# Kernel optimization log

Hardware: AMD Instinct MI355X
Metric: run time of the kernel (lower is better)

The kernel has to match this reference:

```python
import jax, jax.numpy as jnp
import numpy as np

NU, NI, E = 100000, 50000, 819200
FIN, H, OUT = 128, 32, 32


def _l2norm(x):
    # F.normalize(x, p=2, dim=-1): divide by max(||x||, 1e-12)
    n = jnp.linalg.norm(x, axis=-1, keepdims=True)
    return x / jnp.maximum(n, 1e-12)


def _sage(x_src, x_dst, src, dst, n_dst, wl, b, wr):
    # PyG SAGEConv(mean aggr, normalize=True):
    # out = l2norm(lin_l(mean_j x_src[j]) + lin_r(x_dst))
    msg = x_src[src]                                   # [E, Fin] gather
    agg = jax.ops.segment_sum(msg, dst, num_segments=n_dst)
    cnt = jax.ops.segment_sum(jnp.ones((src.shape[0],), x_src.dtype), dst,
                              num_segments=n_dst)
    mean = agg / jnp.maximum(cnt, 1.0)[:, None]
    return _l2norm(mean @ wl.T + b + x_dst @ wr.T)


def setup_inputs() -> dict:
    key = jax.random.key(0)
    ks = jax.random.split(key, 24)
    d = {}
    d["x_user"] = jax.random.normal(ks[0], (NU, FIN), jnp.float32)
    d["x_item"] = jax.random.normal(ks[1], (NI, FIN), jnp.float32)
    d["edge_user"] = jax.random.randint(ks[2], (E,), 0, NU, jnp.int32)
    d["edge_item"] = jax.random.randint(ks[3], (E,), 0, NI, jnp.int32)
    i = [4]
    def w(shape):
        a = jax.random.normal(ks[i[0]], shape, jnp.float32) * 0.05
        i[0] += 1
        return a
    d["wl0_ui"] = w((H, FIN)); d["b0_ui"] = w((H,)); d["wr0_ui"] = w((H, FIN))
    d["wl0_iu"] = w((H, FIN)); d["b0_iu"] = w((H,)); d["wr0_iu"] = w((H, FIN))
    d["wl1_ui"] = w((H, H)); d["b1_ui"] = w((H,)); d["wr1_ui"] = w((H, H))
    d["wl1_iu"] = w((H, H)); d["b1_iu"] = w((H,)); d["wr1_iu"] = w((H, H))
    d["wp_user"] = w((OUT, H)); d["bp_user"] = w((OUT,))
    d["wp_item"] = w((OUT, H)); d["bp_item"] = w((OUT,))
    return d


def reference(x_user, x_item, edge_user, edge_item,
              wl0_ui, b0_ui, wr0_ui, wl0_iu, b0_iu, wr0_iu,
              wl1_ui, b1_ui, wr1_ui, wl1_iu, b1_iu, wr1_iu,
              wp_user, bp_user, wp_item, bp_item):
    # layer 0 (inference mode: dropout is identity)
    item1 = jax.nn.relu(_sage(x_user, x_item, edge_user, edge_item, NI,
                              wl0_ui, b0_ui, wr0_ui))
    user1 = jax.nn.relu(_sage(x_item, x_user, edge_item, edge_user, NU,
                              wl0_iu, b0_iu, wr0_iu))
    # layer 1
    item2 = jax.nn.relu(_sage(user1, item1, edge_user, edge_item, NI,
                              wl1_ui, b1_ui, wr1_ui))
    user2 = jax.nn.relu(_sage(item1, user1, edge_item, edge_user, NU,
                              wl1_iu, b1_iu, wr1_iu))
    user_emb = _l2norm(user2 @ wp_user.T + bp_user)
    item_emb = _l2norm(item2 @ wp_item.T + bp_item)
    return (user_emb, item_emb)
```

## Files before the change

### kernel.cpp

```cpp
#include <hip/hip_runtime.h>
#include <hip/hip_fp16.h>

#define NU 100000
#define NI 50000
#define NE 819200
#define FIN 128
#define HH 32

#define NCH 200
#define NBU 98
#define NBI 49

#define G_P0I 6250
#define G_P0U 12500
#define G_P1U 782
#define G_P1I 391


__global__ void cnt1_k(const int4* __restrict__ eu4, const int4* __restrict__ ei4,
                       int* __restrict__ cntU, int* __restrict__ cntI) {
    __shared__ unsigned cnt[128];
    int b = blockIdx.x;
    int c, NB;
    const int4* D;
    int* M;
    if (b < NCH) { c = b; D = eu4; M = cntU; NB = NBU; }
    else         { c = b - NCH; D = ei4; M = cntI; NB = NBI; }
    int tid = threadIdx.x;
    if (tid < 128) cnt[tid] = 0u;
    __syncthreads();
    int base = c * 1024;
#pragma unroll
    for (int it = 0; it < 4; ++it) {
        int4 v = D[base + it * 256 + tid];
        atomicAdd(&cnt[v.x >> 10], 1u);
        atomicAdd(&cnt[v.y >> 10], 1u);
        atomicAdd(&cnt[v.z >> 10], 1u);
        atomicAdd(&cnt[v.w >> 10], 1u);
    }
    __syncthreads();
    for (int i = tid; i < NB; i += 256) M[i * NCH + c] = (int)cnt[i];
}

__global__ __launch_bounds__(1024) void scan2_k(int* __restrict__ aU, int nU,
                                                int* __restrict__ aI, int nI) {
    __shared__ int ts[1024];
    int t = threadIdx.x;
    for (int pass = 0; pass < 2; ++pass) {
        int* a = pass ? aI : aU;
        int n  = pass ? nI : nU;
        int nper = (n + 1023) / 1024;
        int beg = t * nper;
        int end = beg + nper; if (end > n) end = n;
        int s = 0;
        for (int i = beg; i < end; ++i) s += a[i];
        ts[t] = s;
        __syncthreads();
        int incl = s;
        for (int off = 1; off < 1024; off <<= 1) {
            int y = (t >= off) ? ts[t - off] : 0;
            __syncthreads();
            incl += y;
            ts[t] = incl;
            __syncthreads();
        }
        int run = incl - s;
        for (int i = beg; i < end; ++i) { int v = a[i]; a[i] = run; run += v; }
        __syncthreads();
    }
}

__global__ void part_k(const int4* __restrict__ eu4, const int4* __restrict__ ei4,
                       const int* __restrict__ cntU, const int* __restrict__ cntI,
                       int2* __restrict__ partU, int2* __restrict__ partI) {
    __shared__ unsigned cur[128];
    int b = blockIdx.x;
    int c, NB;
    const int4 *D, *P;
    const int* M;
    int2* out;
    if (b < NCH) { c = b; D = eu4; P = ei4; M = cntU; out = partU; NB = NBU; }
    else         { c = b - NCH; D = ei4; P = eu4; M = cntI; out = partI; NB = NBI; }
    int tid = threadIdx.x;
    for (int i = tid; i < NB; i += 256) cur[i] = (unsigned)M[i * NCH + c];
    __syncthreads();
    int base = c * 1024;
#pragma unroll
    for (int it = 0; it < 4; ++it) {
        int4 d = D[base + it * 256 + tid];
        int4 p = P[base + it * 256 + tid];
        unsigned s;
        s = atomicAdd(&cur[d.x >> 10], 1u); out[s] = make_int2(d.x, p.x);
        s = atomicAdd(&cur[d.y >> 10], 1u); out[s] = make_int2(d.y, p.y);
        s = atomicAdd(&cur[d.z >> 10], 1u); out[s] = make_int2(d.z, p.z);
        s = atomicAdd(&cur[d.w >> 10], 1u); out[s] = make_int2(d.w, p.w);
    }
}

__global__ __launch_bounds__(1024) void build_k(const int2* __restrict__ partU,
                                                const int2* __restrict__ partI,
                                                const int* __restrict__ cntU,
                                                const int* __restrict__ cntI,
                                                int* __restrict__ rsU, int* __restrict__ rsI,
                                                int* __restrict__ csrU, int* __restrict__ csrI) {
    __shared__ unsigned dcnt[1024];
    __shared__ unsigned sc_[1024];
    int b = blockIdx.x;
    const int2* part;
    const int* M;
    int *rs, *csr;
    int bi, N, NB;
    if (b < NBU) { bi = b; part = partU; M = cntU; rs = rsU; csr = csrU; N = NU; NB = NBU; }
    else         { bi = b - NBU; part = partI; M = cntI; rs = rsI; csr = csrI; N = NI; NB = NBI; }
    int lo = bi * 1024;
    int bktbase = M[bi * NCH];
    int bktend = (bi + 1 < NB) ? M[(bi + 1) * NCH] : NE;
    int t = threadIdx.x;
    dcnt[t] = 0u;
    __syncthreads();
    for (int j = bktbase + t; j < bktend; j += 1024) {
        int2 p = part[j];
        atomicAdd(&dcnt[p.x - lo], 1u);
    }
    __syncthreads();
    unsigned cme = dcnt[t];
    sc_[t] = cme;
    __syncthreads();
    unsigned incl = cme;
    for (int off = 1; off < 1024; off <<= 1) {
        unsigned y = (t >= off) ? sc_[t - off] : 0u;
        __syncthreads();
        incl += y;
        sc_[t] = incl;
        __syncthreads();
    }
    unsigned excl = incl - cme;
    if (lo + t < N) rs[lo + t] = bktbase + (int)excl;
    if (bi == NB - 1 && t == 0) rs[N] = NE;
    __syncthreads();
    dcnt[t] = excl;
    __syncthreads();
    for (int j = bktbase + t; j < bktend; j += 1024) {
        int2 p = part[j];
        unsigned s = atomicAdd(&dcnt[p.x - lo], 1u);
        csr[bktbase + (int)s] = p.y;
    }
}

__device__ __forceinline__ void proj128_body(const float* __restrict__ X,
                                             const float* __restrict__ Wl,
                                             const float* __restrict__ Wr,
                                             __half* __restrict__ S, float* __restrict__ R,
                                             int N, int vb, float* sW) {
    int tid = threadIdx.x;
#pragma unroll
    for (int it = 0; it < 4; ++it) {
        int idx = it * 512 + tid;
        int col = idx & 63, k = (idx >> 6) * 4;
        const float* src = (col < 32) ? (Wl + col * FIN + k) : (Wr + (col - 32) * FIN + k);
        float4 w = *(const float4*)src;
        sW[(k + 0) * 68 + col] = w.x;
        sW[(k + 1) * 68 + col] = w.y;
        sW[(k + 2) * 68 + col] = w.z;
        sW[(k + 3) * 68 + col] = w.w;
    }
    __syncthreads();
    int ct = tid & 15, nt = tid >> 4;
    int c0 = ct * 4;
    int n0 = vb * 128 + nt * 4;
    int mA = n0 + 0; if (mA >= N) mA = N - 1;
    int mB = n0 + 1; if (mB >= N) mB = N - 1;
    int mC = n0 + 2; if (mC >= N) mC = N - 1;
    int mD = n0 + 3; if (mD >= N) mD = N - 1;
    const float* xA = X + (size_t)mA * FIN;
    const float* xB = X + (size_t)mB * FIN;
    const float* xC = X + (size_t)mC * FIN;
    const float* xD = X + (size_t)mD * FIN;
    float acc[4][4];
#pragma unroll
    for (int j = 0; j < 4; ++j)
#pragma unroll
        for (int i = 0; i < 4; ++i) acc[j][i] = 0.f;
#pragma unroll 4
    for (int k4 = 0; k4 < FIN; k4 += 4) {
        float4 a4 = *(const float4*)(xA + k4);
        float4 b4 = *(const float4*)(xB + k4);
        float4 c4 = *(const float4*)(xC + k4);
        float4 d4 = *(const float4*)(xD + k4);
        float xa[4] = {a4.x, a4.y, a4.z, a4.w};
        float xb[4] = {b4.x, b4.y, b4.z, b4.w};
        float xc[4] = {c4.x, c4.y, c4.z, c4.w};
        float xd[4] = {d4.x, d4.y, d4.z, d4.w};
#pragma unroll
        for (int kk = 0; kk < 4; ++kk) {
            float4 w = *(const float4*)&sW[(k4 + kk) * 68 + c0];
            acc[0][0] += xa[kk] * w.x; acc[0][1] += xa[kk] * w.y;
            acc[0][2] += xa[kk] * w.z; acc[0][3] += xa[kk] * w.w;
            acc[1][0] += xb[kk] * w.x; acc[1][1] += xb[kk] * w.y;
            acc[1][2] += xb[kk] * w.z; acc[1][3] += xb[kk] * w.w;
            acc[2][0] += xc[kk] * w.x; acc[2][1] += xc[kk] * w.y;
            acc[2][2] += xc[kk] * w.z; acc[2][3] += xc[kk] * w.w;
            acc[3][0] += xd[kk] * w.x; acc[3][1] += xd[kk] * w.y;
            acc[3][2] += xd[kk] * w.z; acc[3][3] += xd[kk] * w.w;
        }
    }
#pragma unroll
    for (int j = 0; j < 4; ++j) {
        int node = n0 + j;
        if (node < N) {
            if (c0 < 32) {
                __half2 h01 = __floats2half2_rn(acc[j][0], acc[j][1]);
                __half2 h23 = __floats2half2_rn(acc[j][2], acc[j][3]);
                __half2* dst = (__half2*)(S + (size_t)node * HH + c0);
                dst[0] = h01;
                dst[1] = h23;
            } else {
                float4 o;
                o.x = acc[j][0]; o.y = acc[j][1]; o.z = acc[j][2]; o.w = acc[j][3];
                *(float4*)(R + (size_t)node * HH + (c0 - 32)) = o;
            }
        }
    }
}

__global__ __launch_bounds__(512) void p1_k(const float* __restrict__ xu,
                                            const float* __restrict__ xi,
                                            const float* __restrict__ wl0_ui,
                                            const float* __restrict__ wr0_iu,
                                            const float* __restrict__ wl0_iu,
                                            const float* __restrict__ wr0_ui,
                                            __half* __restrict__ Su, float* __restrict__ Ru,
                                            __half* __restrict__ Si, float* __restrict__ Ri) {
    __shared__ float sW[128 * 68];
    int b = blockIdx.x;
    if (b < G_P1U) proj128_body(xu, wl0_ui, wr0_iu, Su, Ru, NU, b, sW);
    else           proj128_body(xi, wl0_iu, wr0_ui, Si, Ri, NI, b - G_P1U, sW);
}

__device__ __forceinline__ float4 gather4(const int* __restrict__ csr, int s0, int s1,
                                          const __half* __restrict__ S, int sc, int eh) {
    const char* Sb = (const char*)S;
    float4 acc = {0.f, 0.f, 0.f, 0.f};
    int j = s0 + eh;
    for (; j + 4 < s1; j += 8) {
        int i0 = csr[j], i1 = csr[j + 4];
        uint2 u0 = *(const uint2*)(Sb + ((size_t)i0 << 6) + sc * 8);
        uint2 u1 = *(const uint2*)(Sb + ((size_t)i1 << 6) + sc * 8);
        float2 f00 = __half22float2(*(__half2*)&u0.x);
        float2 f01 = __half22float2(*(__half2*)&u0.y);
        float2 f10 = __half22float2(*(__half2*)&u1.x);
        float2 f11 = __half22float2(*(__half2*)&u1.y);
        acc.x += f00.x + f10.x;
        acc.y += f00.y + f10.y;
        acc.z += f01.x + f11.x;
        acc.w += f01.y + f11.y;
    }
    if (j < s1) {
        int i0 = csr[j];
        uint2 u0 = *(const uint2*)(Sb + ((size_t)i0 << 6) + sc * 8);
        float2 f00 = __half22float2(*(__half2*)&u0.x);
        float2 f01 = __half22float2(*(__half2*)&u0.y);
        acc.x += f00.x; acc.y += f00.y; acc.z += f01.x; acc.w += f01.y;
    }
    acc.x += __shfl_xor(acc.x, 8);  acc.x += __shfl_xor(acc.x, 16);
    acc.y += __shfl_xor(acc.y, 8);  acc.y += __shfl_xor(acc.y, 16);
    acc.z += __shfl_xor(acc.z, 8);  acc.z += __shfl_xor(acc.z, 16);
    acc.w += __shfl_xor(acc.w, 8);  acc.w += __shfl_xor(acc.w, 16);
    return acc;
}

__global__ void p23_k(const int* __restrict__ csrI, const int* __restrict__ rsI,
                      const __half* __restrict__ Su, float* __restrict__ Ri,
                      const float* __restrict__ b0_ui,
                      const float* __restrict__ wl1_iu, const float* __restrict__ wr1_ui,
                      __half* __restrict__ Si2,
                      const int* __restrict__ csrU, const int* __restrict__ rsU,
                      const __half* __restrict__ Si, float* __restrict__ Ru,
                      const float* __restrict__ b0_iu,
                      const float* __restrict__ wl1_ui, const float* __restrict__ wr1_iu,
                      __half* __restrict__ Su2) {
    __shared__ float sWl[HH * 36];
    __shared__ float sWr[HH * 36];
    __shared__ float sH[8][36];
    int b = blockIdx.x;
    const int *csr, *rs;
    const __half* S;
    const float *bias, *Wl, *Wr;
    float* Rb;
    __half* S2;
    int vb;
    if (b < G_P0I) {
        csr = csrI; rs = rsI; S = Su; Rb = Ri; bias = b0_ui;
        Wl = wl1_iu; Wr = wr1_ui; S2 = Si2; vb = b;
    } else {
        csr = csrU; rs = rsU; S = Si; Rb = Ru; bias = b0_iu;
        Wl = wl1_ui; Wr = wr1_iu; S2 = Su2; vb = b - G_P0I;
    }
    int tid = threadIdx.x;
    {
        float4 a = ((const float4*)Wl)[tid];
        float4 w = ((const float4*)Wr)[tid];
        int e0 = tid * 4;
        int o = e0 >> 5, k = e0 & 31;
        sWl[(k + 0) * 36 + o] = a.x;
        sWl[(k + 1) * 36 + o] = a.y;
        sWl[(k + 2) * 36 + o] = a.z;
        sWl[(k + 3) * 36 + o] = a.w;
        sWr[(k + 0) * 36 + o] = w.x;
        sWr[(k + 1) * 36 + o] = w.y;
        sWr[(k + 2) * 36 + o] = w.z;
        sWr[(k + 3) * 36 + o] = w.w;
    }
    int g = tid >> 5;
    int lane5 = tid & 31;
    int sc = lane5 & 7, eh = lane5 >> 3;
    int n = vb * 8 + g;
    int s0 = rs[n], s1 = rs[n + 1];
    float4 acc = gather4(csr, s0, s1, S, sc, eh);
    float deg = (float)(s1 - s0);
    deg = deg > 1.f ? deg : 1.f;
    float4 r4 = *(const float4*)(Rb + (size_t)n * HH + 4 * sc);
    float4 b4 = *(const float4*)(bias + 4 * sc);
    float4 v4;
    v4.x = acc.x / deg + r4.x + b4.x;
    v4.y = acc.y / deg + r4.y + b4.y;
    v4.z = acc.z / deg + r4.z + b4.z;
    v4.w = acc.w / deg + r4.w + b4.w;
    float ss = v4.x * v4.x + v4.y * v4.y + v4.z * v4.z + v4.w * v4.w;
    ss += __shfl_xor(ss, 1);
    ss += __shfl_xor(ss, 2);
    ss += __shfl_xor(ss, 4);
    float nrm = sqrtf(ss);
    nrm = nrm > 1e-12f ? nrm : 1e-12f;
    v4.x /= nrm; v4.y /= nrm; v4.z /= nrm; v4.w /= nrm;
    v4.x = v4.x > 0.f ? v4.x : 0.f;
    v4.y = v4.y > 0.f ? v4.y : 0.f;
    v4.z = v4.z > 0.f ? v4.z : 0.f;
    v4.w = v4.w > 0.f ? v4.w : 0.f;
    if (eh == 0) {
        sH[g][4 * sc + 0] = v4.x;
        sH[g][4 * sc + 1] = v4.y;
        sH[g][4 * sc + 2] = v4.z;
        sH[g][4 * sc + 3] = v4.w;
    }
    __syncthreads();
    int c = tid & 31;
    float aL = 0.f, aR = 0.f;
#pragma unroll
    for (int k = 0; k < HH; ++k) {
        float x = sH[g][k];
        aL += x * sWl[k * 36 + c];
        aR += x * sWr[k * 36 + c];
    }
    S2[(size_t)n * HH + c] = __float2half_rn(aL);
    Rb[(size_t)n * HH + c] = aR;
}

__device__ __forceinline__ void pull1f_body(const int* __restrict__ csr,
                                            const int* __restrict__ rs,
                                            const __half* __restrict__ S,
                                            const float* __restrict__ R,
                                            const float* __restrict__ b1,
                                            const float* __restrict__ Wp,
                                            const float* __restrict__ bp,
                                            float* __restrict__ out, int vb, float* smem) {
    float* sWpT = smem;
    float* sH   = smem + HH * 36;
    int tid = threadIdx.x;
    {
        float4 a = ((const float4*)Wp)[tid];
        int e0 = tid * 4;
        int o = e0 >> 5, k = e0 & 31;
        sWpT[(k + 0) * 36 + o] = a.x;
        sWpT[(k + 1) * 36 + o] = a.y;
        sWpT[(k + 2) * 36 + o] = a.z;
        sWpT[(k + 3) * 36 + o] = a.w;
    }
    int g = tid >> 5;
    int lane5 = tid & 31;
    int sc = lane5 & 7, eh = lane5 >> 3;
    int n = vb * 8 + g;
    int s0 = rs[n], s1 = rs[n + 1];
    float4 acc = gather4(csr, s0, s1, S, sc, eh);
    float deg = (float)(s1 - s0);
    deg = deg > 1.f ? deg : 1.f;
    float4 r4 = *(const float4*)(R + (size_t)n * HH + 4 * sc);
    float4 b4 = *(const float4*)(b1 + 4 * sc);
    float4 v4;
    v4.x = acc.x / deg + r4.x + b4.x;
    v4.y = acc.y / deg + r4.y + b4.y;
    v4.z = acc.z / deg + r4.z + b4.z;
    v4.w = acc.w / deg + r4.w + b4.w;
    float ss = v4.x * v4.x + v4.y * v4.y + v4.z * v4.z + v4.w * v4.w;
    ss += __shfl_xor(ss, 1);
    ss += __shfl_xor(ss, 2);
    ss += __shfl_xor(ss, 4);
    float nrm = sqrtf(ss);
    nrm = nrm > 1e-12f ? nrm : 1e-12f;
    v4.x /= nrm; v4.y /= nrm; v4.z /= nrm; v4.w /= nrm;
    v4.x = v4.x > 0.f ? v4.x : 0.f;
    v4.y = v4.y > 0.f ? v4.y : 0.f;
    v4.z = v4.z > 0.f ? v4.z : 0.f;
    v4.w = v4.w > 0.f ? v4.w : 0.f;
    if (eh == 0) {
        sH[g * 36 + 4 * sc + 0] = v4.x;
        sH[g * 36 + 4 * sc + 1] = v4.y;
        sH[g * 36 + 4 * sc + 2] = v4.z;
        sH[g * 36 + 4 * sc + 3] = v4.w;
    }
    __syncthreads();
    int c = tid & 31;
    float a2f = bp[c];
#pragma unroll
    for (int k = 0; k < HH; ++k) a2f += sH[g * 36 + k] * sWpT[k * 36 + c];
    float s2 = a2f * a2f;
    s2 += __shfl_xor(s2, 1);
    s2 += __shfl_xor(s2, 2);
    s2 += __shfl_xor(s2, 4);
    s2 += __shfl_xor(s2, 8);
    s2 += __shfl_xor(s2, 16);
    float nrm2 = sqrtf(s2);
    nrm2 = nrm2 > 1e-12f ? nrm2 : 1e-12f;
    out[(size_t)n * HH + c] = a2f / nrm2;
}

__global__ void p4_k(const int* __restrict__ csrU, const int* __restrict__ rsU,
                     const __half* __restrict__ Si2, const float* __restrict__ Ru,
                     const float* __restrict__ b1_iu,
                     const float* __restrict__ wp_user, const float* __restrict__ bp_user,
                     const int* __restrict__ csrI, const int* __restrict__ rsI,
                     const __half* __restrict__ Su2, const float* __restrict__ Ri,
                     const float* __restrict__ b1_ui,
                     const float* __restrict__ wp_item, const float* __restrict__ bp_item,
                     float* __restrict__ out) {
    __shared__ float smem[HH * 36 + 8 * 36];
    int b = blockIdx.x;
    if (b < G_P0U) {
        pull1f_body(csrU, rsU, Si2, Ru, b1_iu, wp_user, bp_user, out, b, smem);
    } else {
        pull1f_body(csrI, rsI, Su2, Ri, b1_ui, wp_item, bp_item,
                    out + (size_t)NU * HH, b - G_P0U, smem);
    }
}


extern "C" void kernel_launch(void* const* d_in, const int* in_sizes, int n_in,
                              void* d_out, int out_size, void* d_ws, size_t ws_size,
                              hipStream_t stream) {
    const float* x_user = (const float*)d_in[0];
    const float* x_item = (const float*)d_in[1];
    const int* eu = (const int*)d_in[2];
    const int* ei = (const int*)d_in[3];
    const float* wl0_ui = (const float*)d_in[4];
    const float* b0_ui  = (const float*)d_in[5];
    const float* wr0_ui = (const float*)d_in[6];
    const float* wl0_iu = (const float*)d_in[7];
    const float* b0_iu  = (const float*)d_in[8];
    const float* wr0_iu = (const float*)d_in[9];
    const float* wl1_ui = (const float*)d_in[10];
    const float* b1_ui  = (const float*)d_in[11];
    const float* wr1_ui = (const float*)d_in[12];
    const float* wl1_iu = (const float*)d_in[13];
    const float* b1_iu  = (const float*)d_in[14];
    const float* wr1_iu = (const float*)d_in[15];
    const float* wp_user = (const float*)d_in[16];
    const float* bp_user = (const float*)d_in[17];
    const float* wp_item = (const float*)d_in[18];
    const float* bp_item = (const float*)d_in[19];
    float* out = (float*)d_out;
    (void)in_sizes; (void)n_in; (void)out_size; (void)ws_size;

    char* base = (char*)d_ws;
    size_t off = 0;
    auto take = [&](size_t bytes) -> size_t {
        size_t o = off;
        off += (bytes + 255) & ~(size_t)255;
        return o;
    };
    size_t o_rsU  = take((size_t)(NU + 1) * 4);
    size_t o_rsI  = take((size_t)(NI + 1) * 4);
    size_t o_cntU = take((size_t)NBU * NCH * 4);
    size_t o_cntI = take((size_t)NBI * NCH * 4);
    size_t o_csrU = take((size_t)NE * 4);
    size_t o_csrI = take((size_t)NE * 4);
    size_t o_partU = take((size_t)NE * 8);
    size_t o_partI = take((size_t)NE * 8);
    size_t o_Su = take((size_t)NU * HH * 2);
    size_t o_Si = take((size_t)NI * HH * 2);
    size_t o_Su2 = take((size_t)NU * HH * 2);
    size_t o_Si2 = take((size_t)NI * HH * 2);
    size_t o_Ru = take((size_t)NU * HH * 4);
    size_t o_Ri = take((size_t)NI * HH * 4);

    int* rsU  = (int*)(base + o_rsU);
    int* rsI  = (int*)(base + o_rsI);
    int* cntU = (int*)(base + o_cntU);
    int* cntI = (int*)(base + o_cntI);
    int* csrU = (int*)(base + o_csrU);
    int* csrI = (int*)(base + o_csrI);
    int2* partU = (int2*)(base + o_partU);
    int2* partI = (int2*)(base + o_partI);
    __half* Su = (__half*)(base + o_Su);
    __half* Si = (__half*)(base + o_Si);
    __half* Su2 = (__half*)(base + o_Su2);
    __half* Si2 = (__half*)(base + o_Si2);
    float* Ru = (float*)(base + o_Ru);
    float* Ri = (float*)(base + o_Ri);

    cnt1_k<<<2 * NCH, 256, 0, stream>>>((const int4*)eu, (const int4*)ei, cntU, cntI);
    scan2_k<<<1, 1024, 0, stream>>>(cntU, NBU * NCH, cntI, NBI * NCH);
    part_k<<<2 * NCH, 256, 0, stream>>>((const int4*)eu, (const int4*)ei,
                                        cntU, cntI, partU, partI);
    build_k<<<NBU + NBI, 1024, 0, stream>>>(partU, partI, cntU, cntI,
                                            rsU, rsI, csrU, csrI);

    p1_k<<<G_P1U + G_P1I, 512, 0, stream>>>(x_user, x_item, wl0_ui, wr0_iu,
                                            wl0_iu, wr0_ui, Su, Ru, Si, Ri);

    p23_k<<<G_P0I + G_P0U, 256, 0, stream>>>(csrI, rsI, Su, Ri, b0_ui, wl1_iu, wr1_ui, Si2,
                                             csrU, rsU, Si, Ru, b0_iu, wl1_ui, wr1_iu, Su2);

    p4_k<<<G_P0U + G_P0I, 256, 0, stream>>>(csrU, rsU, Si2, Ru, b1_iu, wp_user, bp_user,
                                            csrI, rsI, Su2, Ri, b1_ui, wp_item, bp_item,
                                            out);
}
```

Baseline: 223.1 us.

## Use MFMA fp16 instructions for layer-0 feature projection

Replaces the scalar FP32 shared-memory tiled projection (X @ [Wl;Wr]^T for 128-dim inputs) with a wave-per-16-row-tile kernel using mfma_f32_16x16x32_f16. Weights are held in registers as fp16 fragments and waves grid-stride over row tiles, with no shared memory or block sync. The projection is memory-bound on reading 150k x 128 floats, so the gain depends on how well the loads are issued. Inputs and weights are now rounded to fp16 before the multiply, which lowers precision, and the output stores become scattered scalar writes.

```diff
diff --git a/kernel.cpp b/kernel.cpp
--- a/kernel.cpp
+++ b/kernel.cpp
@@ -13,8 +13,11 @@
 
 #define G_P0I 6250
 #define G_P0U 12500
-#define G_P1U 782
-#define G_P1I 391
+#define GPU_B 640
+#define GPI_B 320
+
+typedef _Float16 f16x8 __attribute__((ext_vector_type(8)));
+typedef float f32x4 __attribute__((ext_vector_type(4)));
 
 
 __global__ void cnt1_k(const int4* __restrict__ eu4, const int4* __restrict__ ei4,
@@ -147,94 +150,86 @@
     }
 }
 
-__device__ __forceinline__ void proj128_body(const float* __restrict__ X,
-                                             const float* __restrict__ Wl,
-                                             const float* __restrict__ Wr,
-                                             __half* __restrict__ S, float* __restrict__ R,
-                                             int N, int vb, float* sW) {
-    int tid = threadIdx.x;
-#pragma unroll
-    for (int it = 0; it < 4; ++it) {
-        int idx = it * 512 + tid;
-        int col = idx & 63, k = (idx >> 6) * 4;
-        const float* src = (col < 32) ? (Wl + col * FIN + k) : (Wr + (col - 32) * FIN + k);
-        float4 w = *(const float4*)src;
-        sW[(k + 0) * 68 + col] = w.x;
-        sW[(k + 1) * 68 + col] = w.y;
-        sW[(k + 2) * 68 + col] = w.z;
-        sW[(k + 3) * 68 + col] = w.w;
-    }
-    __syncthreads();
-    int ct = tid & 15, nt = tid >> 4;
-    int c0 = ct * 4;
-    int n0 = vb * 128 + nt * 4;
-    int mA = n0 + 0; if (mA >= N) mA = N - 1;
-    int mB = n0 + 1; if (mB >= N) mB = N - 1;
-    int mC = n0 + 2; if (mC >= N) mC = N - 1;
-    int mD = n0 + 3; if (mD >= N) mD = N - 1;
-    const float* xA = X + (size_t)mA * FIN;
-    const float* xB = X + (size_t)mB * FIN;
-    const float* xC = X + (size_t)mC * FIN;
-    const float* xD = X + (size_t)mD * FIN;
-    float acc[4][4];
-#pragma unroll
-    for (int j = 0; j < 4; ++j)
-#pragma unroll
-        for (int i = 0; i < 4; ++i) acc[j][i] = 0.f;
-#pragma unroll 4
-    for (int k4 = 0; k4 < FIN; k4 += 4) {
-        float4 a4 = *(const float4*)(xA + k4);
-        float4 b4 = *(const float4*)(xB + k4);
-        float4 c4 = *(const float4*)(xC + k4);
-        float4 d4 = *(const float4*)(xD + k4);
-        float xa[4] = {a4.x, a4.y, a4.z, a4.w};
-        float xb[4] = {b4.x, b4.y, b4.z, b4.w};
-        float xc[4] = {c4.x, c4.y, c4.z, c4.w};
-        float xd[4] = {d4.x, d4.y, d4.z, d4.w};
-#pragma unroll
-        for (int kk = 0; kk < 4; ++kk) {
-            float4 w = *(const float4*)&sW[(k4 + kk) * 68 + c0];
-            acc[0][0] += xa[kk] * w.x; acc[0][1] += xa[kk] * w.y;
-            acc[0][2] += xa[kk] * w.z; acc[0][3] += xa[kk] * w.w;
-            acc[1][0] += xb[kk] * w.x; acc[1][1] += xb[kk] * w.y;
-            acc[1][2] += xb[kk] * w.z; acc[1][3] += xb[kk] * w.w;
-            acc[2][0] += xc[kk] * w.x; acc[2][1] += xc[kk] * w.y;
-            acc[2][2] += xc[kk] * w.z; acc[2][3] += xc[kk] * w.w;
-            acc[3][0] += xd[kk] * w.x; acc[3][1] += xd[kk] * w.y;
-            acc[3][2] += xd[kk] * w.z; acc[3][3] += xd[kk] * w.w;
+__global__ __launch_bounds__(256) void p1m_k(const float* __restrict__ xu,
+                                             const float* __restrict__ xi,
+                                             const float* __restrict__ wl0_ui,
+                                             const float* __restrict__ wr0_iu,
+                                             const float* __restrict__ wl0_iu,
+                                             const float* __restrict__ wr0_ui,
+                                             __half* __restrict__ Su, float* __restrict__ Ru,
+                                             __half* __restrict__ Si, float* __restrict__ Ri) {
+    const float *X, *Wl, *Wr;
+    __half* S;
+    float* R;
+    int N, nwv, wid;
+    int b = blockIdx.x;
+    if (b < GPU_B) {
+        X = xu; Wl = wl0_ui; Wr = wr0_iu; S = Su; R = Ru; N = NU;
+        nwv = GPU_B * 4; wid = b * 4 + (threadIdx.x >> 6);
+    } else {
+        int bb = b - GPU_B;
+        X = xi; Wl = wl0_iu; Wr = wr0_ui; S = Si; R = Ri; N = NI;
+        nwv = GPI_B * 4; wid = bb * 4 + (threadIdx.x >> 6);
+    }
+    int lane = threadIdx.x & 63;
+    int l15 = lane & 15, kq = lane >> 4;
+    f16x8 bf[4][4];
+#pragma unroll
+    for (int nt = 0; nt < 4; ++nt) {
+        int col = nt * 16 + l15;
+        const float* wrow = (col < 32) ? (Wl + (size_t)col * FIN)
+                                       : (Wr + (size_t)(col - 32) * FIN);
+#pragma unroll
+        for (int ks = 0; ks < 4; ++ks) {
+            int k0 = ks * 32 + kq * 8;
+            float4 wa = *(const float4*)(wrow + k0);
+            float4 wb = *(const float4*)(wrow + k0 + 4);
+            f16x8 v;
+            v[0] = (_Float16)wa.x; v[1] = (_Float16)wa.y;
+            v[2] = (_Float16)wa.z; v[3] = (_Float16)wa.w;
+            v[4] = (_Float16)wb.x; v[5] = (_Float16)wb.y;
+            v[6] = (_Float16)wb.z; v[7] = (_Float16)wb.w;
+            bf[ks][nt] = v;
         }
     }
-#pragma unroll
-    for (int j = 0; j < 4; ++j) {
-        int node = n0 + j;
-        if (node < N) {
-            if (c0 < 32) {
-                __half2 h01 = __floats2half2_rn(acc[j][0], acc[j][1]);
-                __half2 h23 = __floats2half2_rn(acc[j][2], acc[j][3]);
-                __half2* dst = (__half2*)(S + (size_t)node * HH + c0);
-                dst[0] = h01;
-                dst[1] = h23;
-            } else {
-                float4 o;
-                o.x = acc[j][0]; o.y = acc[j][1]; o.z = acc[j][2]; o.w = acc[j][3];
-                *(float4*)(R + (size_t)node * HH + (c0 - 32)) = o;
+    int tiles = (N + 15) >> 4;
+    for (int t = wid; t < tiles; t += nwv) {
+        int row = t * 16 + l15;
+        if (row >= N) row = N - 1;
+        const float* xrow = X + (size_t)row * FIN;
+        f32x4 a0 = {0.f, 0.f, 0.f, 0.f};
+        f32x4 a1 = {0.f, 0.f, 0.f, 0.f};
+        f32x4 a2 = {0.f, 0.f, 0.f, 0.f};
+        f32x4 a3 = {0.f, 0.f, 0.f, 0.f};
+#pragma unroll
+        for (int ks = 0; ks < 4; ++ks) {
+            int k0 = ks * 32 + kq * 8;
+            float4 xa = *(const float4*)(xrow + k0);
+            float4 xb = *(const float4*)(xrow + k0 + 4);
+            f16x8 af;
+            af[0] = (_Float16)xa.x; af[1] = (_Float16)xa.y;
+            af[2] = (_Float16)xa.z; af[3] = (_Float16)xa.w;
+            af[4] = (_Float16)xb.x; af[5] = (_Float16)xb.y;
+            af[6] = (_Float16)xb.z; af[7] = (_Float16)xb.w;
+            a0 = __builtin_amdgcn_mfma_f32_16x16x32_f16(af, bf[ks][0], a0, 0, 0, 0);
+            a1 = __builtin_amdgcn_mfma_f32_16x16x32_f16(af, bf[ks][1], a1, 0, 0, 0);
+            a2 = __builtin_amdgcn_mfma_f32_16x16x32_f16(af, bf[ks][2], a2, 0, 0, 0);
+            a3 = __builtin_amdgcn_mfma_f32_16x16x32_f16(af, bf[ks][3], a3, 0, 0, 0);
+        }
+        int rbase = t * 16 + kq * 4;
+#pragma unroll
+        for (int r = 0; r < 4; ++r) {
+            int node = rbase + r;
+            if (node < N) {
+                _Float16* srow = (_Float16*)(S + (size_t)node * HH);
+                srow[l15]      = (_Float16)a0[r];
+                srow[16 + l15] = (_Float16)a1[r];
+                float* rrow = R + (size_t)node * HH;
+                rrow[l15]      = a2[r];
+                rrow[16 + l15] = a3[r];
             }
         }
     }
-}
-
-__global__ __launch_bounds__(512) void p1_k(const float* __restrict__ xu,
-                                            const float* __restrict__ xi,
-                                            const float* __restrict__ wl0_ui,
-                                            const float* __restrict__ wr0_iu,
-                                            const float* __restrict__ wl0_iu,
-                                            const float* __restrict__ wr0_ui,
-                                            __half* __restrict__ Su, float* __restrict__ Ru,
-                                            __half* __restrict__ Si, float* __restrict__ Ri) {
-    __shared__ float sW[128 * 68];
-    int b = blockIdx.x;
-    if (b < G_P1U) proj128_body(xu, wl0_ui, wr0_iu, Su, Ru, NU, b, sW);
-    else           proj128_body(xi, wl0_iu, wr0_ui, Si, Ri, NI, b - G_P1U, sW);
 }
 
 __device__ __forceinline__ float4 gather4(const int* __restrict__ csr, int s0, int s1,
@@ -514,8 +509,8 @@
     build_k<<<NBU + NBI, 1024, 0, stream>>>(partU, partI, cntU, cntI,
                                             rsU, rsI, csrU, csrI);
 
-    p1_k<<<G_P1U + G_P1I, 512, 0, stream>>>(x_user, x_item, wl0_ui, wr0_iu,
-                                            wl0_iu, wr0_ui, Su, Ru, Si, Ri);
+    p1m_k<<<GPU_B + GPI_B, 256, 0, stream>>>(x_user, x_item, wl0_ui, wr0_iu,
+                                             wl0_iu, wr0_ui, Su, Ru, Si, Ri);
 
     p23_k<<<G_P0I + G_P0U, 256, 0, stream>>>(csrI, rsI, Su, Ri, b0_ui, wl1_iu, wr1_ui, Si2,
                                              csrU, rsU, Si, Ru, b0_iu, wl1_ui, wr1_iu, Su2);
```

Result: faster. 199.9 us (-10.4%).
